# Performance work log

Hardware: AMD Instinct MI355X
Metric: run time of the kernel (lower is better)

## Reference

```python
import jax, jax.numpy as jnp
import numpy as np

H = 1024          # h_dim
FF = 4 * H
E = 8             # num_expert
TOP_K = 2


def setup_inputs() -> dict:
    key = jax.random.key(0)
    ks = jax.random.split(key, 7)
    B, S = 4, 2048
    s = 0.02
    return {
        "x": jax.random.normal(ks[0], (B, S, H), dtype=jnp.float32),
        "Wg": jax.random.normal(ks[1], (H, E), dtype=jnp.float32) * s,
        "bg": jnp.zeros((E,), dtype=jnp.float32),
        "W1": jax.random.normal(ks[2], (E, H, FF), dtype=jnp.float32) * s,
        "b1": jnp.zeros((E, FF), dtype=jnp.float32),
        "W2": jax.random.normal(ks[3], (E, FF, H), dtype=jnp.float32) * s,
        "b2": jnp.zeros((E, H), dtype=jnp.float32),
    }


def _moe(x, Wg, bg, W1, b1, W2, b2):
    B, S, h = x.shape
    hs = x.reshape(-1, h)                                  # [T, H]
    logits = hs @ Wg + bg                                  # [T, E]
    probs = jax.nn.softmax(logits.astype(jnp.float32), axis=-1)
    w, idx = jax.lax.top_k(probs, TOP_K)                   # [T, K]
    w = jax.nn.softmax(w, axis=-1).astype(x.dtype)         # renormalize over top-k
    out = jnp.zeros_like(hs)
    for e in range(E):
        # per-token combine weight for expert e (0 if not selected)
        w_e = jnp.sum(w * (idx == e), axis=-1)             # [T]
        y = jax.nn.relu(hs @ W1[e] + b1[e]) @ W2[e] + b2[e]  # [T, H]
        out = out + w_e[:, None] * y
    return out.reshape(B, S, h), logits


def reference(x, Wg, bg, W1, b1, W2, b2):
    return _moe(x, Wg, bg, W1, b1, W2, b2)
```

## Files before the change

### kernel.cpp

```cpp
#include <hip/hip_runtime.h>
#include <hip/hip_bf16.h>

#define T_TOKENS 8192
#define HD 1024
#define FF 4096
#define NEXP 8
#define NR_MAX 17408

typedef __attribute__((ext_vector_type(8))) short bf16x8;
typedef __attribute__((ext_vector_type(4))) float f32x4;
typedef unsigned short ushort8v __attribute__((ext_vector_type(8)));

static __device__ __forceinline__ float b2f(ushort u) {
    union { unsigned u; float f; } c; c.u = ((unsigned)u) << 16; return c.f;
}
static __device__ __forceinline__ ushort f2b(float f) {
    union { float f; unsigned u; } c; c.f = f;
    unsigned r = c.u + 0x7fffu + ((c.u >> 16) & 1u);
    return (ushort)(r >> 16);
}

__global__ __launch_bounds__(256) void gate_w1t_kernel(
    const float* __restrict__ x, const float* __restrict__ Wg, const float* __restrict__ bg,
    float* __restrict__ logits, int* __restrict__ counts,
    int* __restrict__ e0a, int* __restrict__ e1a,
    float* __restrict__ w0a, float* __restrict__ w1a,
    const float* __restrict__ W1, ushort* __restrict__ W1T)
{
    __shared__ float tile[64][65];
    if (blockIdx.x < 2048) {
        int t = blockIdx.x * 4 + (threadIdx.x >> 6);
        int l = threadIdx.x & 63;
        const float* xr = x + (size_t)t * HD;
        float acc[8] = {0,0,0,0,0,0,0,0};
        #pragma unroll
        for (int i = 0; i < 4; ++i) {
            int h0 = i * 256 + l * 4;
            float4 xv = *(const float4*)(xr + h0);
            #pragma unroll
            for (int j = 0; j < 4; ++j) {
                float xs = (&xv.x)[j];
                const float4* wr = (const float4*)(Wg + (size_t)(h0 + j) * NEXP);
                float4 wa = wr[0], wb = wr[1];
                acc[0] = fmaf(xs, wa.x, acc[0]);
                acc[1] = fmaf(xs, wa.y, acc[1]);
                acc[2] = fmaf(xs, wa.z, acc[2]);
                acc[3] = fmaf(xs, wa.w, acc[3]);
                acc[4] = fmaf(xs, wb.x, acc[4]);
                acc[5] = fmaf(xs, wb.y, acc[5]);
                acc[6] = fmaf(xs, wb.z, acc[6]);
                acc[7] = fmaf(xs, wb.w, acc[7]);
            }
        }
        #pragma unroll
        for (int off = 32; off > 0; off >>= 1) {
            #pragma unroll
            for (int e = 0; e < 8; ++e) acc[e] += __shfl_down(acc[e], off, 64);
        }
        if (l == 0) {
            float lg[8];
            #pragma unroll
            for (int e = 0; e < 8; ++e) {
                lg[e] = acc[e] + bg[e];
                logits[(size_t)t * NEXP + e] = lg[e];
            }
            float m = lg[0];
            #pragma unroll
            for (int e = 1; e < 8; ++e) m = fmaxf(m, lg[e]);
            float p[8], s = 0.f;
            #pragma unroll
            for (int e = 0; e < 8; ++e) { p[e] = expf(lg[e] - m); s += p[e]; }
            float inv = 1.f / s;
            #pragma unroll
            for (int e = 0; e < 8; ++e) p[e] *= inv;
            int i0 = 0;
            #pragma unroll
            for (int e = 1; e < 8; ++e) if (p[e] > p[i0]) i0 = e;
            int i1 = (i0 == 0) ? 1 : 0;
            #pragma unroll
            for (int e = 0; e < 8; ++e) if (e != i0 && p[e] > p[i1]) i1 = e;
            float ed = expf(p[i1] - p[i0]);
            float w0 = 1.f / (1.f + ed);
            float w1 = ed / (1.f + ed);
            e0a[t] = i0; e1a[t] = i1; w0a[t] = w0; w1a[t] = w1;
            atomicAdd(&counts[i0], 1);
            atomicAdd(&counts[i1], 1);
        }
    } else {
        int bb = blockIdx.x - 2048;
        int e = bb >> 10, tid2 = bb & 1023;
        const float* in = W1 + (size_t)e * HD * FF;
        ushort* out = W1T + (size_t)e * HD * FF;
        int R = HD, C = FF;
        int rt = tid2 >> 6, ct = tid2 & 63;
        int r0 = rt * 64, c0 = ct * 64;

        int tr = threadIdx.x >> 4;
        int tc = (threadIdx.x & 15) * 4;
        #pragma unroll
        for (int i = 0; i < 4; ++i) {
            int r = tr + i * 16;
            float4 v = *(const float4*)(in + (size_t)(r0 + r) * C + c0 + tc);
            tile[r][tc + 0] = v.x;
            tile[r][tc + 1] = v.y;
            tile[r][tc + 2] = v.z;
            tile[r][tc + 3] = v.w;
        }
        __syncthreads();
        int cc = threadIdx.x >> 3;
        int rr = (threadIdx.x & 7) * 8;
        #pragma unroll
        for (int i = 0; i < 2; ++i) {
            int c = cc + i * 32;
            ushort8v o;
            #pragma unroll
            for (int j = 0; j < 8; ++j) o[j] = f2b(tile[rr + j][c]);
            *(ushort8v*)(out + (size_t)(c0 + c) * R + r0 + rr) = o;
        }
    }
}

__global__ __launch_bounds__(256) void assign_kernel(
    const int* __restrict__ e0a, const int* __restrict__ e1a,
    const int* __restrict__ counts, int* __restrict__ fill, int* __restrict__ offg,
    int* __restrict__ row0, int* __restrict__ row1, int* __restrict__ row_token)
{
    __shared__ int off[9];
    if (threadIdx.x == 0) {
        int o = 0;
        #pragma unroll
        for (int e = 0; e < 8; ++e) { off[e] = o; o += (counts[e] + 127) & ~127; }
        off[8] = o;
        if (blockIdx.x == 0) {
            #pragma unroll
            for (int i = 0; i < 9; ++i) offg[i] = off[i];
        }
    }
    __syncthreads();
    int t = blockIdx.x * 256 + threadIdx.x;
    if (t >= T_TOKENS) return;
    int e0 = e0a[t];
    int r0 = off[e0] + atomicAdd(&fill[e0], 1);
    row0[t] = r0; row_token[r0] = t;
    int e1 = e1a[t];
    int r1 = off[e1] + atomicAdd(&fill[e1], 1);
    row1[t] = r1; row_token[r1] = t;
}

__global__ __launch_bounds__(256) void gather_kernel(
    const float* __restrict__ x, const int* __restrict__ row_token, ushort* __restrict__ Xp)
{
    int r = blockIdx.x * 2 + (threadIdx.x >> 7);
    int c = (threadIdx.x & 127) * 8;
    int tok = row_token[r];
    ushort8v o;
    if (tok >= 0 && tok < T_TOKENS) {
        const float* src = x + (size_t)tok * HD + c;
        float4 v1 = *(const float4*)(src);
        float4 v2 = *(const float4*)(src + 4);
        o[0] = f2b(v1.x); o[1] = f2b(v1.y); o[2] = f2b(v1.z); o[3] = f2b(v1.w);
        o[4] = f2b(v2.x); o[5] = f2b(v2.y); o[6] = f2b(v2.z); o[7] = f2b(v2.w);
    } else {
        o = (ushort8v){0,0,0,0,0,0,0,0};
    }
    *(ushort8v*)(Xp + (size_t)r * HD + c) = o;
}

__global__ __launch_bounds__(256, 4) void gemm1_w2t_kernel(
    const ushort* __restrict__ A, const ushort* __restrict__ Bt,
    const float* __restrict__ bias, ushort* __restrict__ Out,
    const int* __restrict__ off,
    const float* __restrict__ W2, ushort* __restrict__ W2T)
{
    constexpr int K = HD, NTOT = FF;
    constexpr int NT = NTOT / 128;
    constexpr int NWG = (FF / 128) * (NR_MAX / 128);
    __shared__ __align__(16) char smem[32768];

    if (blockIdx.x < NWG) {
        ushort* L = (ushort*)smem;
        constexpr int chunkc = NWG >> 3;
        int cid = blockIdx.x & 7, q = blockIdx.x >> 3;
        constexpr int mloc = chunkc / NT;
        int mtile = cid * mloc + q % mloc;
        int ntile = q / mloc;
        int r0 = mtile * 128;
        int total = off[8];
        if (r0 >= total) return;
        int e = 0;
        #pragma unroll
        for (int qq = 0; qq < 7; ++qq) if (r0 >= off[qq + 1]) e = qq + 1;

        int tid = threadIdx.x;
        int w = tid >> 6, lane = tid & 63;
        int wr = w >> 1, wc = w & 1;
        int lr = lane & 15, lk = lane >> 4;

        const ushort* Ab = A + (size_t)r0 * K;
        const ushort* Bb = Bt + ((size_t)e * NTOT + (size_t)ntile * 128) * K;

        auto stage = [&](const ushort* gbase, ushort* ldsbase) {
            #pragma unroll
            for (int issue = 0; issue < 2; ++issue) {
                int row = issue * 64 + w * 16 + (lane >> 2);
                int chunk = (lane & 3) ^ ((lane >> 3) & 3);
                const ushort* g = gbase + (size_t)row * K + chunk * 8;
                ushort* lp = ldsbase + (issue * 64 + w * 16) * 32;
                __builtin_amdgcn_global_load_lds(
                    (const __attribute__((address_space(1))) void*)g,
                    (__attribute__((address_space(3))) void*)lp, 16, 0, 0);
            }
        };

        stage(Ab, L + 0 * 4096);
        stage(Bb, L + 1 * 4096);

        f32x4 acc[4][4];
        #pragma unroll
        for (int mi = 0; mi < 4; ++mi)
            #pragma unroll
            for (int ni = 0; ni < 4; ++ni) acc[mi][ni] = (f32x4){0.f, 0.f, 0.f, 0.f};

        __syncthreads();

        constexpr int KT = K / 32;
        int cur = 0;
        int slot = lk ^ ((lr >> 1) & 3);
        for (int kt = 0; kt < KT; ++kt) {
            if (kt + 1 < KT) {
                stage(Ab + (kt + 1) * 32, L + ((cur ^ 1) * 2 + 0) * 4096);
                stage(Bb + (kt + 1) * 32, L + ((cur ^ 1) * 2 + 1) * 4096);
            }
            const ushort* As = L + (cur * 2 + 0) * 4096;
            const ushort* Bs = L + (cur * 2 + 1) * 4096;
            bf16x8 a[4], b[4];
            #pragma unroll
            for (int mi = 0; mi < 4; ++mi)
                a[mi] = *(const bf16x8*)(As + (wr * 64 + mi * 16 + lr) * 32 + slot * 8);
            #pragma unroll
            for (int ni = 0; ni < 4; ++ni)
                b[ni] = *(const bf16x8*)(Bs + (wc * 64 + ni * 16 + lr) * 32 + slot * 8);
            #pragma unroll
            for (int mi = 0; mi < 4; ++mi)
                #pragma unroll
                for (int ni = 0; ni < 4; ++ni)
                    acc[mi][ni] = __builtin_amdgcn_mfma_f32_16x16x32_bf16(
                        a[mi], b[ni], acc[mi][ni], 0, 0, 0);
            __syncthreads();
            cur ^= 1;
        }

        int c0 = ntile * 128 + wc * 64;
        int rbase = r0 + wr * 64;
        #pragma unroll
        for (int ni = 0; ni < 4; ++ni) {
            int n = c0 + ni * 16 + lr;
            float bv = bias[(size_t)e * NTOT + n];
            #pragma unroll
            for (int mi = 0; mi < 4; ++mi) {
                int m = rbase + mi * 16 + lk * 4;
                #pragma unroll
                for (int j = 0; j < 4; ++j) {
                    float v = acc[mi][ni][j] + bv;
                    v = fmaxf(v, 0.f);
                    Out[(size_t)(m + j) * NTOT + n] = f2b(v);
                }
            }
        }
    } else {
        float (*tile)[65] = (float(*)[65])smem;
        int bb = blockIdx.x - NWG;
        int e = bb >> 10, tid2 = bb & 1023;
        const float* in = W2 + (size_t)e * FF * HD;
        ushort* out = W2T + (size_t)e * FF * HD;
        int R = FF, C = HD;
        int rt = tid2 >> 4, ct = tid2 & 15;
        int r0 = rt * 64, c0 = ct * 64;

        int tr = threadIdx.x >> 4;
        int tc = (threadIdx.x & 15) * 4;
        #pragma unroll
        for (int i = 0; i < 4; ++i) {
            int r = tr + i * 16;
            float4 v = *(const float4*)(in + (size_t)(r0 + r) * C + c0 + tc);
            tile[r][tc + 0] = v.x;
            tile[r][tc + 1] = v.y;
            tile[r][tc + 2] = v.z;
            tile[r][tc + 3] = v.w;
        }
        __syncthreads();
        int cc = threadIdx.x >> 3;
        int rr = (threadIdx.x & 7) * 8;
        #pragma unroll
        for (int i = 0; i < 2; ++i) {
            int c = cc + i * 32;
            ushort8v o;
            #pragma unroll
            for (int j = 0; j < 8; ++j) o[j] = f2b(tile[rr + j][c]);
            *(ushort8v*)(out + (size_t)(c0 + c) * R + r0 + rr) = o;
        }
    }
}

template<int K, int NTOT, bool RELU, bool MFAST>
__global__ __launch_bounds__(256, 4) void gemm_kernel(
    const ushort* __restrict__ A, const ushort* __restrict__ Bt,
    const float* __restrict__ bias, ushort* __restrict__ Out,
    const int* __restrict__ off)
{
    constexpr int NT = NTOT / 128;
    __shared__ __align__(16) ushort lds[2][2][128 * 32];

    int nwg = gridDim.x;
    int chunkc = nwg >> 3;
    int cid = blockIdx.x & 7, q = blockIdx.x >> 3;
    int mtile, ntile;
    if constexpr (MFAST) {
        int mloc = chunkc / NT;
        mtile = cid * mloc + q % mloc;
        ntile = q / mloc;
    } else {
        int wgid = cid * chunkc + q;
        ntile = wgid % NT;
        mtile = wgid / NT;
    }
    int r0 = mtile * 128;
    int total = off[8];
    if (r0 >= total) return;
    int e = 0;
    #pragma unroll
    for (int qq = 0; qq < 7; ++qq) if (r0 >= off[qq + 1]) e = qq + 1;

    int tid = threadIdx.x;
    int w = tid >> 6, lane = tid & 63;
    int wr = w >> 1, wc = w & 1;
    int lr = lane & 15, lk = lane >> 4;

    const ushort* Ab = A + (size_t)r0 * K;
    const ushort* Bb = Bt + ((size_t)e * NTOT + (size_t)ntile * 128) * K;

    auto stage = [&](const ushort* gbase, ushort* ldsbase) {
        #pragma unroll
        for (int issue = 0; issue < 2; ++issue) {
            int row = issue * 64 + w * 16 + (lane >> 2);
            int chunk = (lane & 3) ^ ((lane >> 3) & 3);
            const ushort* g = gbase + (size_t)row * K + chunk * 8;
            ushort* lp = ldsbase + (issue * 64 + w * 16) * 32;
            __builtin_amdgcn_global_load_lds(
                (const __attribute__((address_space(1))) void*)g,
                (__attribute__((address_space(3))) void*)lp, 16, 0, 0);
        }
    };

    stage(Ab, &lds[0][0][0]);
    stage(Bb, &lds[0][1][0]);

    f32x4 acc[4][4];
    #pragma unroll
    for (int mi = 0; mi < 4; ++mi)
        #pragma unroll
        for (int ni = 0; ni < 4; ++ni) acc[mi][ni] = (f32x4){0.f, 0.f, 0.f, 0.f};

    __syncthreads();

    constexpr int KT = K / 32;
    int cur = 0;
    int slot = lk ^ ((lr >> 1) & 3);
    for (int kt = 0; kt < KT; ++kt) {
        if (kt + 1 < KT) {
            stage(Ab + (kt + 1) * 32, &lds[cur ^ 1][0][0]);
            stage(Bb + (kt + 1) * 32, &lds[cur ^ 1][1][0]);
        }
        const ushort* As = &lds[cur][0][0];
        const ushort* Bs = &lds[cur][1][0];
        bf16x8 a[4], b[4];
        #pragma unroll
        for (int mi = 0; mi < 4; ++mi)
            a[mi] = *(const bf16x8*)(As + (wr * 64 + mi * 16 + lr) * 32 + slot * 8);
        #pragma unroll
        for (int ni = 0; ni < 4; ++ni)
            b[ni] = *(const bf16x8*)(Bs + (wc * 64 + ni * 16 + lr) * 32 + slot * 8);
        #pragma unroll
        for (int mi = 0; mi < 4; ++mi)
            #pragma unroll
            for (int ni = 0; ni < 4; ++ni)
                acc[mi][ni] = __builtin_amdgcn_mfma_f32_16x16x32_bf16(
                    a[mi], b[ni], acc[mi][ni], 0, 0, 0);
        __syncthreads();
        cur ^= 1;
    }

    int c0 = ntile * 128 + wc * 64;
    int rbase = r0 + wr * 64;
    #pragma unroll
    for (int ni = 0; ni < 4; ++ni) {
        int n = c0 + ni * 16 + lr;
        float bv = bias[(size_t)e * NTOT + n];
        #pragma unroll
        for (int mi = 0; mi < 4; ++mi) {
            int m = rbase + mi * 16 + lk * 4;
            #pragma unroll
            for (int j = 0; j < 4; ++j) {
                float v = acc[mi][ni][j] + bv;
                if (RELU) v = fmaxf(v, 0.f);
                Out[(size_t)(m + j) * NTOT + n] = f2b(v);
            }
        }
    }
}

__global__ __launch_bounds__(256) void combine_kernel(
    const ushort* __restrict__ Y, const int* __restrict__ row0, const int* __restrict__ row1,
    const float* __restrict__ w0a, const float* __restrict__ w1a, float* __restrict__ out)
{
    int t = blockIdx.x;
    int c = threadIdx.x * 4;
    int r0 = row0[t], r1 = row1[t];
    float w0 = w0a[t], w1 = w1a[t];
    ushort4 ya = *(const ushort4*)(Y + (size_t)r0 * HD + c);
    ushort4 yb = *(const ushort4*)(Y + (size_t)r1 * HD + c);
    float4 o;
    o.x = w0 * b2f(ya.x) + w1 * b2f(yb.x);
    o.y = w0 * b2f(ya.y) + w1 * b2f(yb.y);
    o.z = w0 * b2f(ya.z) + w1 * b2f(yb.z);
    o.w = w0 * b2f(ya.w) + w1 * b2f(yb.w);
    *(float4*)(out + (size_t)t * HD + c) = o;
}

#define WSA(x) (((x) + 255) & ~(size_t)255)
static constexpr size_t OFF_COUNTS = 0;
static constexpr size_t OFF_FILL   = 64;
static constexpr size_t OFF_OFF    = 128;
static constexpr size_t OFF_E0     = 256;
static constexpr size_t OFF_E1     = OFF_E0 + (size_t)T_TOKENS * 4;
static constexpr size_t OFF_W0     = OFF_E1 + (size_t)T_TOKENS * 4;
static constexpr size_t OFF_W1A    = OFF_W0 + (size_t)T_TOKENS * 4;
static constexpr size_t OFF_R0     = OFF_W1A + (size_t)T_TOKENS * 4;
static constexpr size_t OFF_R1     = OFF_R0 + (size_t)T_TOKENS * 4;
static constexpr size_t OFF_RT     = OFF_R1 + (size_t)T_TOKENS * 4;
static constexpr size_t OFF_XP     = WSA(OFF_RT + (size_t)NR_MAX * 4);
static constexpr size_t OFF_W1T    = OFF_XP  + (size_t)NR_MAX * HD * 2;
static constexpr size_t OFF_W2T    = OFF_W1T + (size_t)NEXP * FF * HD * 2;
static constexpr size_t OFF_H1     = OFF_W2T + (size_t)NEXP * HD * FF * 2;
static constexpr size_t OFF_Y      = OFF_H1  + (size_t)NR_MAX * FF * 2;
static constexpr size_t WS_NEEDED  = OFF_Y   + (size_t)NR_MAX * HD * 2;

extern "C" void kernel_launch(void* const* d_in, const int* in_sizes, int n_in,
                              void* d_out, int out_size, void* d_ws, size_t ws_size,
                              hipStream_t stream) {
    (void)in_sizes; (void)n_in; (void)out_size;
    const float* x  = (const float*)d_in[0];
    const float* Wg = (const float*)d_in[1];
    const float* bg = (const float*)d_in[2];
    const float* W1 = (const float*)d_in[3];
    const float* b1 = (const float*)d_in[4];
    const float* W2 = (const float*)d_in[5];
    const float* b2 = (const float*)d_in[6];
    float* out    = (float*)d_out;
    float* logits = out + (size_t)T_TOKENS * HD;

    if (ws_size < WS_NEEDED) return;

    char* ws = (char*)d_ws;
    int*    counts = (int*)(ws + OFF_COUNTS);
    int*    fill   = (int*)(ws + OFF_FILL);
    int*    offp   = (int*)(ws + OFF_OFF);
    int*    e0a    = (int*)(ws + OFF_E0);
    int*    e1a    = (int*)(ws + OFF_E1);
    float*  w0a    = (float*)(ws + OFF_W0);
    float*  w1a    = (float*)(ws + OFF_W1A);
    int*    row0   = (int*)(ws + OFF_R0);
    int*    row1   = (int*)(ws + OFF_R1);
    int*    rowtok = (int*)(ws + OFF_RT);
    ushort* Xp     = (ushort*)(ws + OFF_XP);
    ushort* W1T    = (ushort*)(ws + OFF_W1T);
    ushort* W2T    = (ushort*)(ws + OFF_W2T);
    ushort* H1     = (ushort*)(ws + OFF_H1);
    ushort* Y      = (ushort*)(ws + OFF_Y);

    hipMemsetAsync(ws, 0, 256, stream);
    hipMemsetAsync(rowtok, 0xFF, (size_t)NR_MAX * 4, stream);

    gate_w1t_kernel<<<2048 + 8192, 256, 0, stream>>>(
        x, Wg, bg, logits, counts, e0a, e1a, w0a, w1a, W1, W1T);
    assign_kernel<<<T_TOKENS / 256, 256, 0, stream>>>(e0a, e1a, counts, fill, offp, row0, row1, rowtok);
    gather_kernel<<<NR_MAX / 2, 256, 0, stream>>>(x, rowtok, Xp);
    gemm1_w2t_kernel<<<(FF / 128) * (NR_MAX / 128) + 8192, 256, 0, stream>>>(
        Xp, W1T, b1, H1, offp, W2, W2T);
    gemm_kernel<FF, HD, false, false>
        <<<(HD / 128) * (NR_MAX / 128), 256, 0, stream>>>(H1, W2T, b2, Y, offp);
    combine_kernel<<<T_TOKENS, 256, 0, stream>>>(Y, row0, row1, w0a, w1a, out);
}
```

Baseline: 734.1 us.

## Fuse gather into assign and combine into GEMM2 epilogue via atomic scatter

Routing assignment and the bf16 gather of x are merged into one token-major kernel. Each token row of x is read once and written to both of its expert slots, and a per-row combine weight is stored. The combine kernel and the bf16 Y buffer are removed: the second GEMM epilogue scales each accumulator by its row weight and atomically adds it into the zeroed fp32 output at the owning token's position. This drops a full Y round trip and one launch, at the cost of an extra output memset and many scattered float atomics. Padding rows of Xp are no longer zeroed, but their results are skipped in the scatter.

Result: slower. 911.0 us (+24.1%).

```diff
diff --git a/kernel.cpp b/kernel.cpp
--- a/kernel.cpp
+++ b/kernel.cpp
@@ -120,12 +120,15 @@
     }
 }
 
-__global__ __launch_bounds__(256) void assign_kernel(
+__global__ __launch_bounds__(256) void assign_gather_kernel(
+    const float* __restrict__ x,
     const int* __restrict__ e0a, const int* __restrict__ e1a,
+    const float* __restrict__ w0a, const float* __restrict__ w1a,
     const int* __restrict__ counts, int* __restrict__ fill, int* __restrict__ offg,
-    int* __restrict__ row0, int* __restrict__ row1, int* __restrict__ row_token)
+    int* __restrict__ row_token, float* __restrict__ wrow, ushort* __restrict__ Xp)
 {
     __shared__ int off[9];
+    __shared__ int rshare[2][2];
     if (threadIdx.x == 0) {
         int o = 0;
         #pragma unroll
@@ -137,33 +140,27 @@
         }
     }
     __syncthreads();
-    int t = blockIdx.x * 256 + threadIdx.x;
-    if (t >= T_TOKENS) return;
-    int e0 = e0a[t];
-    int r0 = off[e0] + atomicAdd(&fill[e0], 1);
-    row0[t] = r0; row_token[r0] = t;
-    int e1 = e1a[t];
-    int r1 = off[e1] + atomicAdd(&fill[e1], 1);
-    row1[t] = r1; row_token[r1] = t;
-}
-
-__global__ __launch_bounds__(256) void gather_kernel(
-    const float* __restrict__ x, const int* __restrict__ row_token, ushort* __restrict__ Xp)
-{
-    int r = blockIdx.x * 2 + (threadIdx.x >> 7);
-    int c = (threadIdx.x & 127) * 8;
-    int tok = row_token[r];
+    int half = threadIdx.x >> 7;
+    int lane = threadIdx.x & 127;
+    int t = blockIdx.x * 2 + half;
+    if (lane == 0) {
+        int e0 = e0a[t];
+        int r0 = off[e0] + atomicAdd(&fill[e0], 1);
+        row_token[r0] = t; wrow[r0] = w0a[t]; rshare[half][0] = r0;
+        int e1 = e1a[t];
+        int r1 = off[e1] + atomicAdd(&fill[e1], 1);
+        row_token[r1] = t; wrow[r1] = w1a[t]; rshare[half][1] = r1;
+    }
+    __syncthreads();
+    int r0 = rshare[half][0], r1 = rshare[half][1];
+    const float* src = x + (size_t)t * HD + lane * 8;
+    float4 v1 = *(const float4*)(src);
+    float4 v2 = *(const float4*)(src + 4);
     ushort8v o;
-    if (tok >= 0 && tok < T_TOKENS) {
-        const float* src = x + (size_t)tok * HD + c;
-        float4 v1 = *(const float4*)(src);
-        float4 v2 = *(const float4*)(src + 4);
-        o[0] = f2b(v1.x); o[1] = f2b(v1.y); o[2] = f2b(v1.z); o[3] = f2b(v1.w);
-        o[4] = f2b(v2.x); o[5] = f2b(v2.y); o[6] = f2b(v2.z); o[7] = f2b(v2.w);
-    } else {
-        o = (ushort8v){0,0,0,0,0,0,0,0};
-    }
-    *(ushort8v*)(Xp + (size_t)r * HD + c) = o;
+    o[0] = f2b(v1.x); o[1] = f2b(v1.y); o[2] = f2b(v1.z); o[3] = f2b(v1.w);
+    o[4] = f2b(v2.x); o[5] = f2b(v2.y); o[6] = f2b(v2.z); o[7] = f2b(v2.w);
+    *(ushort8v*)(Xp + (size_t)r0 * HD + lane * 8) = o;
+    *(ushort8v*)(Xp + (size_t)r1 * HD + lane * 8) = o;
 }
 
 __global__ __launch_bounds__(256, 4) void gemm1_w2t_kernel(
@@ -302,28 +299,22 @@
     }
 }
 
-template<int K, int NTOT, bool RELU, bool MFAST>
-__global__ __launch_bounds__(256, 4) void gemm_kernel(
+__global__ __launch_bounds__(256, 4) void gemm2_scatter_kernel(
     const ushort* __restrict__ A, const ushort* __restrict__ Bt,
-    const float* __restrict__ bias, ushort* __restrict__ Out,
-    const int* __restrict__ off)
+    const float* __restrict__ bias,
+    const int* __restrict__ rowtok, const float* __restrict__ wrow,
+    float* __restrict__ out, const int* __restrict__ off)
 {
+    constexpr int K = FF, NTOT = HD;
     constexpr int NT = NTOT / 128;
     __shared__ __align__(16) ushort lds[2][2][128 * 32];
 
     int nwg = gridDim.x;
     int chunkc = nwg >> 3;
     int cid = blockIdx.x & 7, q = blockIdx.x >> 3;
-    int mtile, ntile;
-    if constexpr (MFAST) {
-        int mloc = chunkc / NT;
-        mtile = cid * mloc + q % mloc;
-        ntile = q / mloc;
-    } else {
-        int wgid = cid * chunkc + q;
-        ntile = wgid % NT;
-        mtile = wgid / NT;
-    }
+    int wgid = cid * chunkc + q;
+    int ntile = wgid % NT;
+    int mtile = wgid / NT;
     int r0 = mtile * 128;
     int total = off[8];
     if (r0 >= total) return;
@@ -390,41 +381,32 @@
         cur ^= 1;
     }
 
+    int* toks = (int*)&lds[0][0][0];
+    float* wvs = (float*)(&lds[0][0][0] + 4096);
+    if (tid < 128) {
+        toks[tid] = rowtok[r0 + tid];
+        wvs[tid]  = wrow[r0 + tid];
+    }
+    __syncthreads();
+
     int c0 = ntile * 128 + wc * 64;
-    int rbase = r0 + wr * 64;
     #pragma unroll
     for (int ni = 0; ni < 4; ++ni) {
         int n = c0 + ni * 16 + lr;
         float bv = bias[(size_t)e * NTOT + n];
         #pragma unroll
         for (int mi = 0; mi < 4; ++mi) {
-            int m = rbase + mi * 16 + lk * 4;
+            int mloc = wr * 64 + mi * 16 + lk * 4;
             #pragma unroll
             for (int j = 0; j < 4; ++j) {
-                float v = acc[mi][ni][j] + bv;
-                if (RELU) v = fmaxf(v, 0.f);
-                Out[(size_t)(m + j) * NTOT + n] = f2b(v);
-            }
-        }
-    }
-}
-
-__global__ __launch_bounds__(256) void combine_kernel(
-    const ushort* __restrict__ Y, const int* __restrict__ row0, const int* __restrict__ row1,
-    const float* __restrict__ w0a, const float* __restrict__ w1a, float* __restrict__ out)
-{
-    int t = blockIdx.x;
-    int c = threadIdx.x * 4;
-    int r0 = row0[t], r1 = row1[t];
-    float w0 = w0a[t], w1 = w1a[t];
-    ushort4 ya = *(const ushort4*)(Y + (size_t)r0 * HD + c);
-    ushort4 yb = *(const ushort4*)(Y + (size_t)r1 * HD + c);
-    float4 o;
-    o.x = w0 * b2f(ya.x) + w1 * b2f(yb.x);
-    o.y = w0 * b2f(ya.y) + w1 * b2f(yb.y);
-    o.z = w0 * b2f(ya.z) + w1 * b2f(yb.z);
-    o.w = w0 * b2f(ya.w) + w1 * b2f(yb.w);
-    *(float4*)(out + (size_t)t * HD + c) = o;
+                int tok = toks[mloc + j];
+                if (tok >= 0) {
+                    float v = wvs[mloc + j] * (acc[mi][ni][j] + bv);
+                    atomicAdd(&out[(size_t)tok * HD + n], v);
+                }
+            }
+        }
+    }
 }
 
 #define WSA(x) (((x) + 255) & ~(size_t)255)
@@ -435,15 +417,13 @@
 static constexpr size_t OFF_E1     = OFF_E0 + (size_t)T_TOKENS * 4;
 static constexpr size_t OFF_W0     = OFF_E1 + (size_t)T_TOKENS * 4;
 static constexpr size_t OFF_W1A    = OFF_W0 + (size_t)T_TOKENS * 4;
-static constexpr size_t OFF_R0     = OFF_W1A + (size_t)T_TOKENS * 4;
-static constexpr size_t OFF_R1     = OFF_R0 + (size_t)T_TOKENS * 4;
-static constexpr size_t OFF_RT     = OFF_R1 + (size_t)T_TOKENS * 4;
-static constexpr size_t OFF_XP     = WSA(OFF_RT + (size_t)NR_MAX * 4);
+static constexpr size_t OFF_RT     = OFF_W1A + (size_t)T_TOKENS * 4;
+static constexpr size_t OFF_WROW   = OFF_RT + (size_t)NR_MAX * 4;
+static constexpr size_t OFF_XP     = WSA(OFF_WROW + (size_t)NR_MAX * 4);
 static constexpr size_t OFF_W1T    = OFF_XP  + (size_t)NR_MAX * HD * 2;
 static constexpr size_t OFF_W2T    = OFF_W1T + (size_t)NEXP * FF * HD * 2;
 static constexpr size_t OFF_H1     = OFF_W2T + (size_t)NEXP * HD * FF * 2;
-static constexpr size_t OFF_Y      = OFF_H1  + (size_t)NR_MAX * FF * 2;
-static constexpr size_t WS_NEEDED  = OFF_Y   + (size_t)NR_MAX * HD * 2;
+static constexpr size_t WS_NEEDED  = OFF_H1  + (size_t)NR_MAX * FF * 2;
 
 extern "C" void kernel_launch(void* const* d_in, const int* in_sizes, int n_in,
                               void* d_out, int out_size, void* d_ws, size_t ws_size,
@@ -469,25 +449,23 @@
     int*    e1a    = (int*)(ws + OFF_E1);
     float*  w0a    = (float*)(ws + OFF_W0);
     float*  w1a    = (float*)(ws + OFF_W1A);
-    int*    row0   = (int*)(ws + OFF_R0);
-    int*    row1   = (int*)(ws + OFF_R1);
     int*    rowtok = (int*)(ws + OFF_RT);
+    float*  wrow   = (float*)(ws + OFF_WROW);
     ushort* Xp     = (ushort*)(ws + OFF_XP);
     ushort* W1T    = (ushort*)(ws + OFF_W1T);
     ushort* W2T    = (ushort*)(ws + OFF_W2T);
     ushort* H1     = (ushort*)(ws + OFF_H1);
-    ushort* Y      = (ushort*)(ws + OFF_Y);
 
     hipMemsetAsync(ws, 0, 256, stream);
     hipMemsetAsync(rowtok, 0xFF, (size_t)NR_MAX * 4, stream);
+    hipMemsetAsync(out, 0, (size_t)T_TOKENS * HD * 4, stream);
 
     gate_w1t_kernel<<<2048 + 8192, 256, 0, stream>>>(
         x, Wg, bg, logits, counts, e0a, e1a, w0a, w1a, W1, W1T);
-    assign_kernel<<<T_TOKENS / 256, 256, 0, stream>>>(e0a, e1a, counts, fill, offp, row0, row1, rowtok);
-    gather_kernel<<<NR_MAX / 2, 256, 0, stream>>>(x, rowtok, Xp);
+    assign_gather_kernel<<<T_TOKENS / 2, 256, 0, stream>>>(
+        x, e0a, e1a, w0a, w1a, counts, fill, offp, rowtok, wrow, Xp);
     gemm1_w2t_kernel<<<(FF / 128) * (NR_MAX / 128) + 8192, 256, 0, stream>>>(
         Xp, W1T, b1, H1, offp, W2, W2T);
-    gemm_kernel<FF, HD, false, false>
-        <<<(HD / 128) * (NR_MAX / 128), 256, 0, stream>>>(H1, W2T, b2, Y, offp);
-    combine_kernel<<<T_TOKENS, 256, 0, stream>>>(Y, row0, row1, w0a, w1a, out);
-}
+    gemm2_scatter_kernel<<<(HD / 128) * (NR_MAX / 128), 256, 0, stream>>>(
+        H1, W2T, b2, rowtok, wrow, out, offp);
+}
```
